# Kernel tuning notes

Hardware: AMD Instinct MI355X
Metric: run time of the kernel (lower is better)

## Reference

```python
import jax, jax.numpy as jnp
import numpy as np

B, P, T = 32, 196, 32           # batch, num pixels (14*14), seq_len
E, H, A, V = 512, 512, 256, 30000  # embed, hidden, attention, vocab
FEAT = 2048

def _ln(x, g, b, eps=1e-5):
    m = jnp.mean(x, -1, keepdims=True)
    v = jnp.mean((x - m) ** 2, -1, keepdims=True)
    return (x - m) / jnp.sqrt(v + eps) * g + b

def setup_inputs() -> dict:
    key = jax.random.key(0)
    ks = iter(jax.random.split(key, 32))
    def rn(shape, s=0.05):
        return (jax.random.normal(next(ks), shape, dtype=jnp.float32) * s)
    inp = {
        'features': jax.random.normal(next(ks), (B, P, FEAT), dtype=jnp.float32),
        'captions': jax.random.randint(next(ks), (B, T), 0, V),
        # feature adapter Linear(2048->E) + LayerNorm
        'Wad': rn((E, FEAT)), 'bad': jnp.zeros((E,), jnp.float32),
        'g_ad': jnp.ones((E,), jnp.float32), 'b_ad': jnp.zeros((E,), jnp.float32),
        # additive attention
        'We': rn((A, E)), 'be': jnp.zeros((A,), jnp.float32),
        'Wd': rn((A, H)), 'bd': jnp.zeros((A,), jnp.float32),
        'Wf': rn((1, A)), 'bf': jnp.zeros((1,), jnp.float32),
        # embedding table (uniform(-0.1,0.1) as in torch init)
        'emb': jax.random.uniform(next(ks), (V, E), jnp.float32, -0.1, 0.1),
        # LSTM layer 0: input 2E, layer 1: input H; gates order i,f,g,o; forget bias 1
        'W_ih0': rn((4 * H, 2 * E)), 'W_hh0': rn((4 * H, H)),
        'b_ih0': jnp.concatenate([jnp.zeros(H), jnp.ones(H), jnp.zeros(2 * H)]).astype(jnp.float32),
        'b_hh0': jnp.zeros((4 * H,), jnp.float32),
        'W_ih1': rn((4 * H, H)), 'W_hh1': rn((4 * H, H)),
        'b_ih1': jnp.concatenate([jnp.zeros(H), jnp.ones(H), jnp.zeros(2 * H)]).astype(jnp.float32),
        'b_hh1': jnp.zeros((4 * H,), jnp.float32),
        # output head
        'W1': rn((H // 2, H)), 'b1': jnp.zeros((H // 2,), jnp.float32),
        'g1': jnp.ones((H // 2,), jnp.float32), 'bb1': jnp.zeros((H // 2,), jnp.float32),
        'W2': rn((V, H // 2)), 'b2': jnp.zeros((V,), jnp.float32),
    }
    return inp

def reference(features, captions, Wad, bad, g_ad, b_ad, We, be, Wd, bd, Wf, bf,
              emb, W_ih0, W_hh0, b_ih0, b_hh0, W_ih1, W_hh1, b_ih1, b_hh1,
              W1, b1, g1, bb1, W2, b2):
    # feature adapter (dropout = identity in eval)
    enc = _ln(jax.nn.relu(features @ Wad.T + bad), g_ad, b_ad)   # [B,P,E]
    att1 = enc @ We.T + be                                        # [B,P,A] (same every step)
    embs = emb[captions]                                          # [B,T,E]

    def lstm_cell(x, h, c, Wih, Whh, bih, bhh):
        gates = x @ Wih.T + bih + h @ Whh.T + bhh                 # [B,4H]
        i, f, g, o = jnp.split(gates, 4, axis=1)
        c_n = jax.nn.sigmoid(f) * c + jax.nn.sigmoid(i) * jnp.tanh(g)
        h_n = jax.nn.sigmoid(o) * jnp.tanh(c_n)
        return h_n, c_n

    def step(carry, emb_t):
        h, c = carry                                              # each [2,B,H]
        # additive attention against top-layer hidden state
        att2 = h[1] @ Wd.T + bd                                   # [B,A]
        e = (jax.nn.relu(att1 + att2[:, None, :]) @ Wf.T + bf)[..., 0]  # [B,P]
        alpha = jax.nn.softmax(e, axis=1)                         # (max-subtract is folded in)
        ctx = jnp.einsum('bp,bpe->be', alpha, enc)                # [B,E]
        x = jnp.concatenate([emb_t, ctx], axis=1)                 # [B,2E]
        h0, c0 = lstm_cell(x,  h[0], c[0], W_ih0, W_hh0, b_ih0, b_hh0)
        h1, c1 = lstm_cell(h0, h[1], c[1], W_ih1, W_hh1, b_ih1, b_hh1)
        out = jax.nn.relu(_ln(h1 @ W1.T + b1, g1, bb1))
        out = jnp.clip(out @ W2.T + b2, -10.0, 10.0)              # [B,V]
        return (jnp.stack([h0, h1]), jnp.stack([c0, c1])), out

    h0 = jnp.zeros((2, B, H), jnp.float32)
    c0 = jnp.zeros((2, B, H), jnp.float32)
    _, outs = jax.lax.scan(step, (h0, c0), jnp.swapaxes(embs, 0, 1))
    return jnp.swapaxes(outs, 0, 1)                               # [B,T,V]
```

## Files before the change

kernel.cpp:

```cpp
#include <hip/hip_runtime.h>

#define B_ 32
#define P_ 196
#define T_ 32
#define E_ 512
#define H_ 512
#define A_ 256
#define V_ 30000
#define FEAT_ 2048

typedef unsigned short u16;
typedef __attribute__((ext_vector_type(8))) short bf16x8;
typedef __attribute__((ext_vector_type(4))) float fx4;

#define MFMA16 __builtin_amdgcn_mfma_f32_16x16x32_bf16

__device__ __forceinline__ u16 f2b(float f){
  unsigned u = __builtin_bit_cast(unsigned, f);
  u += 0x7FFFu + ((u >> 16) & 1u);
  return (u16)(u >> 16);
}
__device__ __forceinline__ float b2f(u16 h){
  unsigned u = ((unsigned)h) << 16;
  return __builtin_bit_cast(float, u);
}
__device__ __forceinline__ float sigm(float x){ return 1.f/(1.f + __expf(-x)); }

#define PREP_BLOCKS 25398
__global__ void k_prep(const float* __restrict__ Wad, const float* __restrict__ We,
                       const float* __restrict__ W1f, const float* __restrict__ W2f,
                       const float* __restrict__ Wd,
                       const float* __restrict__ Wih0, const float* __restrict__ Whh0,
                       const float* __restrict__ Wih1, const float* __restrict__ Whh1,
                       const float* __restrict__ bih0, const float* __restrict__ bhh0,
                       const float* __restrict__ bih1, const float* __restrict__ bhh1,
                       const float* __restrict__ emb, const int* __restrict__ cap,
                       u16* __restrict__ Wad16, u16* __restrict__ We16,
                       u16* __restrict__ W1_16, u16* __restrict__ W2pk,
                       unsigned* __restrict__ Wd2, u16* __restrict__ Wg0pk,
                       u16* __restrict__ W1ppk, float* __restrict__ bias0p,
                       float* __restrict__ bias1p, u16* __restrict__ embs16){
  int bid = blockIdx.x, tid = threadIdx.x;
  if (bid < 12288){
    int eid = bid*256 + tid;
    int j = eid & 7, l = (eid >> 3) & 63, frag = eid >> 9;
    int ks = frag % 12; int rest = frag / 12;
    int kw = rest & 3, q = (rest >> 2) & 3, s = rest >> 4;
    int n = q*512 + s*16 + (l & 15);
    int k = kw*384 + ks*32 + ((l >> 4) << 3) + j;
    float v = (k < 1024) ? Wih0[(size_t)n*1024 + k] : Whh0[(size_t)n*512 + (k - 1024)];
    Wg0pk[eid] = f2b(v);
  } else if (bid < 20480){
    int eid = (bid-12288)*256 + tid;
    int j = eid & 7, l = (eid >> 3) & 63, f = eid >> 9;
    int nf = f & 127, s = f >> 7;
    int np = nf*16 + (l & 15);
    int k = ((l >> 4) << 3) + j;
    int orig = ((np >> 4) & 3)*512 + (np >> 6)*16 + (np & 15);
    float v = (k < 16) ? Wih1[(size_t)orig*512 + s*16 + k]
                       : Whh1[(size_t)orig*512 + s*16 + (k - 16)];
    W1ppk[eid] = f2b(v);
  } else if (bid < 24230){
    int i = (bid-20480)*256 + tid;
    int l = i & 63, kc = (i >> 6) & 7, nf = i >> 9;
    int row = nf*16 + (l & 15);
    int col = kc*32 + (l >> 4)*8;
    const float4* s = (const float4*)(W2f + (size_t)row*256 + col);
    float4 a = s[0], b = s[1];
    ushort4* d = (ushort4*)(W2pk + (size_t)i*8);
    d[0] = make_ushort4(f2b(a.x), f2b(a.y), f2b(a.z), f2b(a.w));
    d[1] = make_ushort4(f2b(b.x), f2b(b.y), f2b(b.z), f2b(b.w));
  } else if (bid < 24742){
    int i = (bid-24230)*256 + tid;
    const float4* s = (const float4*)Wad + (size_t)i*2;
    float4 a = s[0], b = s[1];
    ushort4* d = (ushort4*)Wad16 + (size_t)i*2;
    d[0] = make_ushort4(f2b(a.x), f2b(a.y), f2b(a.z), f2b(a.w));
    d[1] = make_ushort4(f2b(b.x), f2b(b.y), f2b(b.z), f2b(b.w));
  } else if (bid < 24806){
    int i = (bid-24742)*256 + tid;
    const float4* s = (const float4*)We + (size_t)i*2;
    float4 a = s[0], b = s[1];
    ushort4* d = (ushort4*)We16 + (size_t)i*2;
    d[0] = make_ushort4(f2b(a.x), f2b(a.y), f2b(a.z), f2b(a.w));
    d[1] = make_ushort4(f2b(b.x), f2b(b.y), f2b(b.z), f2b(b.w));
  } else if (bid < 24870){
    int i = (bid-24806)*256 + tid;
    const float4* s = (const float4*)W1f + (size_t)i*2;
    float4 a = s[0], b = s[1];
    ushort4* d = (ushort4*)W1_16 + (size_t)i*2;
    d[0] = make_ushort4(f2b(a.x), f2b(a.y), f2b(a.z), f2b(a.w));
    d[1] = make_ushort4(f2b(b.x), f2b(b.y), f2b(b.z), f2b(b.w));
  } else if (bid < 25126){
    int i = (bid-24870)*256 + tid;
    int n = i & 255, kp = i >> 8;
    unsigned lo = f2b(Wd[n*512 + 2*kp]);
    unsigned hi = f2b(Wd[n*512 + 2*kp + 1]);
    Wd2[i] = lo | (hi << 16);
  } else if (bid < 25134){
    int n = (bid-25126)*256 + tid;
    int c = n & 15, q = (n >> 4) & 3, s = n >> 6;
    int orig = q*512 + s*16 + c;
    bias0p[n] = bih0[orig] + bhh0[orig];
  } else if (bid < 25142){
    int n = (bid-25134)*256 + tid;
    int c = n & 15, q = (n >> 4) & 3, s = n >> 6;
    int orig = q*512 + s*16 + c;
    bias1p[n] = bih1[orig] + bhh1[orig];
  } else {
    int r = (bid-25142)*4 + (tid >> 6), l = tid & 63;
    int t = r >> 5, b = r & 31;
    int c = cap[b*T_ + t];
    const float4* s = (const float4*)(emb + (size_t)c*E_) + l*2;
    float4 a = s[0], bb = s[1];
    ushort4* d = (ushort4*)(embs16 + (size_t)r*E_) + l*2;
    d[0] = make_ushort4(f2b(a.x), f2b(a.y), f2b(a.z), f2b(a.w));
    d[1] = make_ushort4(f2b(bb.x), f2b(bb.y), f2b(bb.z), f2b(bb.w));
  }
}

template<int MODE, int BM, int BN, int KS, int NQ>
__launch_bounds__(256)
__global__ void k_gemm(const u16* __restrict__ A, const u16* __restrict__ W,
                       const float* __restrict__ bias, u16* __restrict__ outB,
                       int M, int N, int K){
  constexpr int NI = BN/32, MI = BM/32, SEGS = KS/8;
  __shared__ __align__(16) u16 As[BM][KS+8];
  __shared__ __align__(16) u16 Bs[BN][KS+8];
  int f = blockIdx.x;
  int p8 = f & 7; int rest = f >> 3;
  int q = rest % NQ; int pHigh = rest / NQ;
  int p = pHigh*8 + p8;
  if (p*BM >= M) return;
  int m0 = p*BM, n0 = q*BN;
  int tid = threadIdx.x;
  int l = tid & 63, w = tid >> 6;
  int wr = w >> 1, wc = w & 1;
  fx4 acc[MI][NI];
  #pragma unroll
  for (int i=0;i<MI;i++)
    #pragma unroll
    for (int j=0;j<NI;j++) acc[i][j] = (fx4){0.f,0.f,0.f,0.f};
  int lr = l & 15, lg = l >> 4;
  for (int k0 = 0; k0 < K; k0 += KS){
    #pragma unroll
    for (int it=0; it<BM*SEGS/256; ++it){
      int flat = it*256 + tid, rr = flat/SEGS, cs = (flat%SEGS)*8;
      *(uint4*)&As[rr][cs] = *(const uint4*)(A + (size_t)(m0+rr)*K + k0 + cs);
    }
    uint4 z = {0u,0u,0u,0u};
    #pragma unroll
    for (int it=0; it<BN*SEGS/256; ++it){
      int flat = it*256 + tid, rr = flat/SEGS, cs = (flat%SEGS)*8;
      int rb = n0 + rr;
      *(uint4*)&Bs[rr][cs] = (rb < N) ? *(const uint4*)(W + (size_t)rb*K + k0 + cs) : z;
    }
    __syncthreads();
    #pragma unroll
    for (int kk=0; kk<KS/32; ++kk){
      bf16x8 av[MI], bv[NI];
      #pragma unroll
      for (int mi=0; mi<MI; mi++) av[mi] = *(const bf16x8*)&As[wr*(BM/2) + mi*16 + lr][kk*32 + lg*8];
      #pragma unroll
      for (int ni=0; ni<NI; ni++) bv[ni] = *(const bf16x8*)&Bs[wc*(BN/2) + ni*16 + lr][kk*32 + lg*8];
      #pragma unroll
      for (int mi=0; mi<MI; mi++)
        #pragma unroll
        for (int ni=0; ni<NI; ni++)
          acc[mi][ni] = MFMA16(av[mi], bv[ni], acc[mi][ni], 0, 0, 0);
    }
    __syncthreads();
  }
  #pragma unroll
  for (int mi=0; mi<MI; mi++)
    #pragma unroll
    for (int ni=0; ni<NI; ni++){
      int col = n0 + wc*(BN/2) + ni*16 + lr;
      if (col >= N) continue;
      float bvs = bias[col];
      #pragma unroll
      for (int reg=0; reg<4; reg++){
        int rowm = m0 + wr*(BM/2) + mi*16 + lg*4 + reg;
        float v = acc[mi][ni][reg] + bvs;
        if (MODE == 0) v = fmaxf(v, 0.f);
        outB[(size_t)rowm*N + col] = f2b(v);
      }
    }
}

template<int BM, int BN, int KS, int NQ>
__launch_bounds__(256)
__global__ void k_gemmF(const float* __restrict__ A, const u16* __restrict__ W,
                        const float* __restrict__ bias, u16* __restrict__ outB,
                        int M, int N, int K){
  constexpr int NI = BN/32, MI = BM/32, SEGS = KS/8;
  __shared__ __align__(16) u16 As[BM][KS+8];
  __shared__ __align__(16) u16 Bs[BN][KS+8];
  int f = blockIdx.x;
  int p8 = f & 7; int rest = f >> 3;
  int q = rest % NQ; int pHigh = rest / NQ;
  int p = pHigh*8 + p8;
  if (p*BM >= M) return;
  int m0 = p*BM, n0 = q*BN;
  int tid = threadIdx.x;
  int l = tid & 63, w = tid >> 6;
  int wr = w >> 1, wc = w & 1;
  fx4 acc[MI][NI];
  #pragma unroll
  for (int i=0;i<MI;i++)
    #pragma unroll
    for (int j=0;j<NI;j++) acc[i][j] = (fx4){0.f,0.f,0.f,0.f};
  int lr = l & 15, lg = l >> 4;
  for (int k0 = 0; k0 < K; k0 += KS){
    #pragma unroll
    for (int it=0; it<BM*SEGS/256; ++it){
      int flat = it*256 + tid, rr = flat/SEGS, cs = (flat%SEGS)*8;
      const float4* s = (const float4*)(A + (size_t)(m0+rr)*K + k0 + cs);
      float4 a0 = s[0], a1 = s[1];
      *(ushort4*)&As[rr][cs]   = make_ushort4(f2b(a0.x), f2b(a0.y), f2b(a0.z), f2b(a0.w));
      *(ushort4*)&As[rr][cs+4] = make_ushort4(f2b(a1.x), f2b(a1.y), f2b(a1.z), f2b(a1.w));
    }
    #pragma unroll
    for (int it=0; it<BN*SEGS/256; ++it){
      int flat = it*256 + tid, rr = flat/SEGS, cs = (flat%SEGS)*8;
      *(uint4*)&Bs[rr][cs] = *(const uint4*)(W + (size_t)(n0+rr)*K + k0 + cs);
    }
    __syncthreads();
    #pragma unroll
    for (int kk=0; kk<KS/32; ++kk){
      bf16x8 av[MI], bv[NI];
      #pragma unroll
      for (int mi=0; mi<MI; mi++) av[mi] = *(const bf16x8*)&As[wr*(BM/2) + mi*16 + lr][kk*32 + lg*8];
      #pragma unroll
      for (int ni=0; ni<NI; ni++) bv[ni] = *(const bf16x8*)&Bs[wc*(BN/2) + ni*16 + lr][kk*32 + lg*8];
      #pragma unroll
      for (int mi=0; mi<MI; mi++)
        #pragma unroll
        for (int ni=0; ni<NI; ni++)
          acc[mi][ni] = MFMA16(av[mi], bv[ni], acc[mi][ni], 0, 0, 0);
    }
    __syncthreads();
  }
  #pragma unroll
  for (int mi=0; mi<MI; mi++)
    #pragma unroll
    for (int ni=0; ni<NI; ni++){
      int col = n0 + wc*(BN/2) + ni*16 + lr;
      float bvs = bias[col];
      #pragma unroll
      for (int reg=0; reg<4; reg++){
        int rowm = m0 + wr*(BM/2) + mi*16 + lg*4 + reg;
        float v = fmaxf(acc[mi][ni][reg] + bvs, 0.f);
        outB[(size_t)rowm*N + col] = f2b(v);
      }
    }
}

__global__ void k_ln1(const u16* __restrict__ pre, const float* __restrict__ g,
                      const float* __restrict__ bt, u16* __restrict__ enc){
  int row = blockIdx.x; int l = threadIdx.x;
  bf16x8 vv = *(const bf16x8*)(pre + (size_t)row*E_ + l*8);
  float x[8]; float s = 0.f;
  #pragma unroll
  for (int i=0;i<8;i++){ x[i] = b2f((u16)vv[i]); s += x[i]; }
  #pragma unroll
  for (int off=32; off; off>>=1) s += __shfl_xor(s, off, 64);
  float mean = s * (1.f/512.f);
  float vs = 0.f;
  #pragma unroll
  for (int i=0;i<8;i++){ float d = x[i]-mean; vs += d*d; }
  #pragma unroll
  for (int off=32; off; off>>=1) vs += __shfl_xor(vs, off, 64);
  float inv = rsqrtf(vs*(1.f/512.f) + 1e-5f);
  int c0 = l*8;
  u16 o[8];
  #pragma unroll
  for (int i=0;i<8;i++) o[i] = f2b((x[i]-mean)*inv*g[c0+i] + bt[c0+i]);
  ushort4* d = (ushort4*)(enc + (size_t)row*E_ + c0);
  d[0] = make_ushort4(o[0],o[1],o[2],o[3]);
  d[1] = make_ushort4(o[4],o[5],o[6],o[7]);
}

__device__ __forceinline__ void w1ln_block(const u16* __restrict__ h1all,
    const u16* __restrict__ W1, const float* __restrict__ b1,
    const float* __restrict__ g1v, const float* __restrict__ bb1,
    u16* __restrict__ hid, int u, int tid, float* red2, float* mv){
  int l = tid & 63, w = tid >> 6, lr = l & 15, lg = l >> 4;
  fx4 acc[2] = {{0,0,0,0},{0,0,0,0}};
  for (int k0 = 0; k0 < 512; k0 += 32){
    bf16x8 bv  = *(const bf16x8*)(W1 + (size_t)(w*16+lr)*512 + k0 + lg*8);
    bf16x8 av0 = *(const bf16x8*)(h1all + ((size_t)lr*T_ + u)*512 + k0 + lg*8);
    bf16x8 av1 = *(const bf16x8*)(h1all + ((size_t)(16+lr)*T_ + u)*512 + k0 + lg*8);
    acc[0] = MFMA16(av0, bv, acc[0], 0,0,0);
    acc[1] = MFMA16(av1, bv, acc[1], 0,0,0);
  }
  int col = w*16 + lr;
  float bc = b1[col];
  float val[2][4], s1[2][4], s2[2][4];
  #pragma unroll
  for (int mi=0;mi<2;mi++)
    #pragma unroll
    for (int reg=0;reg<4;reg++){
      float v = acc[mi][reg] + bc;
      val[mi][reg] = v; s1[mi][reg] = v; s2[mi][reg] = v*v;
    }
  #pragma unroll
  for (int off=1; off<16; off<<=1){
    #pragma unroll
    for (int mi=0;mi<2;mi++)
      #pragma unroll
      for (int reg=0;reg<4;reg++){
        s1[mi][reg] += __shfl_xor(s1[mi][reg], off, 64);
        s2[mi][reg] += __shfl_xor(s2[mi][reg], off, 64);
      }
  }
  if (lr == 0){
    #pragma unroll
    for (int mi=0;mi<2;mi++)
      #pragma unroll
      for (int reg=0;reg<4;reg++){
        int row = mi*16 + lg*4 + reg;
        red2[(0*16 + w)*32 + row] = s1[mi][reg];
        red2[(16   + w)*32 + row] = s2[mi][reg];
      }
  }
  __syncthreads();
  if (tid < 64){
    int which = tid >> 5, row = tid & 31;
    float s = 0.f;
    #pragma unroll
    for (int ww=0; ww<16; ++ww) s += red2[(which*16 + ww)*32 + row];
    mv[which*32 + row] = s;
  }
  __syncthreads();
  #pragma unroll
  for (int mi=0;mi<2;mi++)
    #pragma unroll
    for (int reg=0;reg<4;reg++){
      int row = mi*16 + lg*4 + reg;
      float mean = mv[row] * (1.f/256.f);
      float var  = mv[32+row] * (1.f/256.f) - mean*mean;
      float inv  = rsqrtf(var + 1e-5f);
      float o = fmaxf((val[mi][reg]-mean)*inv*g1v[col] + bb1[col], 0.f);
      hid[((size_t)u*32 + row)*256 + col] = f2b(o);
    }
}

__launch_bounds__(1024)
__global__ void k_w1(const u16* __restrict__ h1all, const u16* __restrict__ W1_16,
                     const float* __restrict__ b1, const float* __restrict__ g1v,
                     const float* __restrict__ bb1, u16* __restrict__ hid16){
  __shared__ float red2[1024];
  __shared__ float mv[64];
  w1ln_block(h1all, W1_16, b1, g1v, bb1, hid16, blockIdx.x, threadIdx.x, red2, mv);
}

__launch_bounds__(1024)
__global__ void k_head(const u16* __restrict__ hid, const u16* __restrict__ W2pk,
                       const float* __restrict__ b2, float* __restrict__ out){
  __shared__ __align__(16) union { u16 hA[32][264]; float Cs[32][260]; } S;
  int c = blockIdx.x, uh = blockIdx.y, tid = threadIdx.x;
  int l = tid & 63, w = tid >> 6, lr = l & 15, lg = l >> 4;
  int nf = c*16 + w;
  bool valid = nf < 1875;
  bf16x8 bw[8];
  if (valid){
    const u16* wp = W2pk + (size_t)nf*4096 + l*8;
    #pragma unroll
    for (int k0=0;k0<8;k0++) bw[k0] = *(const bf16x8*)(wp + k0*512);
  }
  int srow = tid >> 5, scc = (tid & 31)*8;
  int col0 = c*256 + scc;
  float bb[8];
  #pragma unroll
  for (int j=0;j<8;j++) bb[j] = (col0 + j < V_) ? b2[col0 + j] : 0.f;

  for (int ui=0; ui<16; ++ui){
    int u = uh*16 + ui;
    { int arow = tid >> 5, ak = (tid & 31)*8;
      *(uint4*)&S.hA[arow][ak] = *(const uint4*)(hid + ((size_t)u*32 + arow)*256 + ak); }
    __syncthreads();
    fx4 acc0 = {0,0,0,0}, acc1 = {0,0,0,0};
    if (valid){
      #pragma unroll
      for (int k0=0;k0<8;k0++){
        bf16x8 av0 = *(const bf16x8*)&S.hA[lr][k0*32 + lg*8];
        bf16x8 av1 = *(const bf16x8*)&S.hA[16+lr][k0*32 + lg*8];
        acc0 = MFMA16(av0, bw[k0], acc0, 0,0,0);
        acc1 = MFMA16(av1, bw[k0], acc1, 0,0,0);
      }
    }
    __syncthreads();
    #pragma unroll
    for (int reg=0; reg<4; ++reg){
      S.Cs[lg*4+reg][w*16+lr]    = acc0[reg];
      S.Cs[16+lg*4+reg][w*16+lr] = acc1[reg];
    }
    __syncthreads();
    if (col0 + 8 <= V_){
      float4 v0, v1;
      v0.x = fminf(fmaxf(S.Cs[srow][scc+0] + bb[0], -10.f), 10.f);
      v0.y = fminf(fmaxf(S.Cs[srow][scc+1] + bb[1], -10.f), 10.f);
      v0.z = fminf(fmaxf(S.Cs[srow][scc+2] + bb[2], -10.f), 10.f);
      v0.w = fminf(fmaxf(S.Cs[srow][scc+3] + bb[3], -10.f), 10.f);
      v1.x = fminf(fmaxf(S.Cs[srow][scc+4] + bb[4], -10.f), 10.f);
      v1.y = fminf(fmaxf(S.Cs[srow][scc+5] + bb[5], -10.f), 10.f);
      v1.z = fminf(fmaxf(S.Cs[srow][scc+6] + bb[6], -10.f), 10.f);
      v1.w = fminf(fmaxf(S.Cs[srow][scc+7] + bb[7], -10.f), 10.f);
      float* o = out + ((size_t)srow*T_ + u)*V_ + col0;
      *(float4*)o = v0; *(float4*)(o+4) = v1;
    }
    __syncthreads();
  }
}

__launch_bounds__(1024)
__global__ void k_ly(const float* __restrict__ part1, const float* __restrict__ bias1p,
                     float* __restrict__ c1buf, u16* __restrict__ h1all,
                     const unsigned* __restrict__ Wd2, const float* __restrict__ bd,
                     const u16* __restrict__ att1b, const u16* __restrict__ enc16,
                     const float* __restrict__ Wf, const float* __restrict__ bfp,
                     const u16* __restrict__ embs, u16* __restrict__ xh0cur, int t){
  int b = blockIdx.x, tid = threadIdx.x;
  int l = tid & 63, wid = tid >> 6;
  __shared__ float g1s[2048];
  __shared__ float h1s[512];
  __shared__ float a2p[4][256];
  __shared__ float a2[256], ev[256], red[8], wfv[256], bdv[256];
  __shared__ float cb[4][256][2];
  if (tid < 256){ wfv[tid] = Wf[tid]; bdv[tid] = bd[tid]; }
  float bf0 = bfp[0];

  if (t > 0){
    float acc0 = bias1p[tid], acc1 = bias1p[tid + 1024];
    #pragma unroll 4
    for (int s2=0; s2<32; ++s2){
      const float* pp = part1 + ((size_t)(s2*32 + b))*2048;
      acc0 += pp[tid];
      acc1 += pp[tid + 1024];
    }
    g1s[tid] = acc0; g1s[tid + 1024] = acc1;
    __syncthreads();
    if (tid < 512){
      int h = tid, s4 = h >> 4, c = h & 15, base = s4*64 + c;
      float gi = g1s[base], gf = g1s[base+16], gg = g1s[base+32], go = g1s[base+48];
      float cold = c1buf[b*512 + h];
      float cn = sigm(gf)*cold + sigm(gi)*tanhf(gg);
      c1buf[b*512 + h] = cn;
      float hn = sigm(go)*tanhf(cn);
      h1s[h] = hn;
      h1all[((size_t)b*T_ + (t-1))*512 + h] = f2b(hn);
    }
  } else {
    if (tid < 512) h1s[tid] = 0.f;
  }
  __syncthreads();
  if (t >= T_) return;

  {
    int n = tid & 255, kq = tid >> 8;
    float acc = 0.f;
    const unsigned* wp = Wd2 + (size_t)kq*64*256 + n;
    #pragma unroll 8
    for (int kp2 = 0; kp2 < 64; ++kp2){
      unsigned wv = wp[(size_t)kp2*256];
      int k0 = (kq*64 + kp2)*2;
      acc += h1s[k0]   * b2f((u16)(wv & 0xFFFFu))
           + h1s[k0+1] * b2f((u16)(wv >> 16));
    }
    a2p[kq][n] = acc;
  }
  __syncthreads();
  if (tid < 256) a2[tid] = a2p[0][tid] + a2p[1][tid] + a2p[2][tid] + a2p[3][tid] + bdv[tid];
  __syncthreads();
  for (int pi = 0; pi < 13; ++pi){
    int p = pi*16 + wid;
    if (p < P_){
      ushort4 av4 = *(const ushort4*)(att1b + (size_t)(b*P_ + p)*A_ + l*4);
      int j0 = l*4;
      float sum = fmaxf(b2f(av4.x)+a2[j0],  0.f)*wfv[j0]
                + fmaxf(b2f(av4.y)+a2[j0+1],0.f)*wfv[j0+1]
                + fmaxf(b2f(av4.z)+a2[j0+2],0.f)*wfv[j0+2]
                + fmaxf(b2f(av4.w)+a2[j0+3],0.f)*wfv[j0+3];
      #pragma unroll
      for (int off=32; off; off>>=1) sum += __shfl_xor(sum, off, 64);
      if (l == 0) ev[p] = sum + bf0;
    }
  }
  __syncthreads();
  if (tid < 256){
    float v = (tid < P_) ? ev[tid] : -1e30f;
    float m = v;
    #pragma unroll
    for (int off=32; off; off>>=1) m = fmaxf(m, __shfl_xor(m, off, 64));
    if (l == 0) red[wid] = m;
  }
  __syncthreads();
  float mg = fmaxf(fmaxf(red[0],red[1]), fmaxf(red[2],red[3]));
  if (tid < 256){
    float ex = (tid < P_) ? __expf(ev[tid] - mg) : 0.f;
    float ss = ex;
    #pragma unroll
    for (int off=32; off; off>>=1) ss += __shfl_xor(ss, off, 64);
    if (l == 0) red[4+wid] = ss;
    ev[tid] = ex;
  }
  __syncthreads();
  float inv = 1.f/(red[4]+red[5]+red[6]+red[7]);
  {
    int j = tid & 255, pq = tid >> 8;
    float A0 = 0.f, A1 = 0.f;
    const unsigned* ep = (const unsigned*)enc16 + ((size_t)b*P_ + pq*49)*256 + j;
    #pragma unroll 7
    for (int pi = 0; pi < 49; ++pi){
      unsigned vv = ep[(size_t)pi*256];
      float al = ev[pq*49 + pi];
      A0 += al * b2f((u16)(vv & 0xFFFFu));
      A1 += al * b2f((u16)(vv >> 16));
    }
    cb[pq][j][0] = A0; cb[pq][j][1] = A1;
  }
  __syncthreads();
  if (tid < 256){
    float c0 = (cb[0][tid][0]+cb[1][tid][0]+cb[2][tid][0]+cb[3][tid][0]) * inv;
    float c1 = (cb[0][tid][1]+cb[1][tid][1]+cb[2][tid][1]+cb[3][tid][1]) * inv;
    unsigned o = (unsigned)f2b(c0) | (((unsigned)f2b(c1)) << 16);
    *((unsigned*)(xh0cur + (size_t)b*1536 + 512) + tid) = o;
    ((unsigned*)(xh0cur + (size_t)b*1536))[tid] =
        ((const unsigned*)(embs + (size_t)(t*32+b)*E_))[tid];
  }
}

__launch_bounds__(1024)
__global__ void k_lx(const u16* __restrict__ xh0cur, u16* __restrict__ xh0nxt,
                     const u16* __restrict__ Wg0pk, const float* __restrict__ bias0p,
                     const u16* __restrict__ W1ppk, const u16* __restrict__ h1all,
                     float* __restrict__ c0buf, float* __restrict__ part1, int t){
  __shared__ float part[16][32][16];
  __shared__ float gsum[4][32][16];
  __shared__ __align__(16) u16 As[32][40];
  int tid = threadIdx.x, s = blockIdx.x;
  int l = tid & 63, kw = tid >> 6, lr = l & 15, lg = l >> 4;

  bf16x8 a[2][3];
  #pragma unroll
  for (int mi=0;mi<2;mi++)
    #pragma unroll
    for (int ks=0;ks<3;ks++)
      a[mi][ks] = *(const bf16x8*)(xh0cur + (size_t)(mi*16+lr)*1536 + kw*96 + ks*32 + lg*8);
  for (int q=0;q<4;q++){
    fx4 acc0 = (fx4){0,0,0,0}, acc1 = (fx4){0,0,0,0};
    const u16* wp = Wg0pk + (size_t)(((s*4+q)*4 + (kw>>2))*12 + (kw&3)*3)*512 + l*8;
    #pragma unroll
    for (int ks=0;ks<3;ks++){
      bf16x8 bf8 = *(const bf16x8*)(wp + ks*512);
      acc0 = MFMA16(a[0][ks], bf8, acc0, 0,0,0);
      acc1 = MFMA16(a[1][ks], bf8, acc1, 0,0,0);
    }
    #pragma unroll
    for (int reg=0;reg<4;reg++){
      part[kw][lg*4+reg][lr]    = acc0[reg];
      part[kw][16+lg*4+reg][lr] = acc1[reg];
    }
    __syncthreads();
    if (tid < 512){
      int bb = tid >> 4, c = tid & 15;
      float g = bias0p[s*64 + q*16 + c];
      #pragma unroll
      for (int kw2=0; kw2<16; ++kw2) g += part[kw2][bb][c];
      gsum[q][bb][c] = g;
    }
    __syncthreads();
  }
  if (tid < 256){
    int bb = tid >> 3, kk = (tid & 7)*2;
    unsigned hv = 0;
    if (t > 0) hv = *(const unsigned*)(h1all + ((size_t)bb*T_ + (t-1))*512 + s*16 + kk);
    *(unsigned*)&As[bb][16+kk] = hv;
  }
  if (tid < 512){
    int bb = tid >> 4, c = tid & 15;
    int h = s*16 + c;
    float gi = gsum[0][bb][c], gf = gsum[1][bb][c], gg = gsum[2][bb][c], go = gsum[3][bb][c];
    float cold = c0buf[bb*512 + h];
    float cn = sigm(gf)*cold + sigm(gi)*tanhf(gg);
    c0buf[bb*512 + h] = cn;
    u16 hb = f2b(sigm(go)*tanhf(cn));
    xh0nxt[(size_t)bb*1536 + 1024 + h] = hb;
    As[bb][c] = hb;
  }
  __syncthreads();
  bf16x8 pa0 = *(const bf16x8*)&As[lr][lg*8];
  bf16x8 pa1 = *(const bf16x8*)&As[16+lr][lg*8];
  #pragma unroll 2
  for (int i=0;i<8;i++){
    int nf = kw*8 + i;
    bf16x8 bf8 = *(const bf16x8*)(W1ppk + (size_t)(s*128 + nf)*512 + l*8);
    fx4 A0 = MFMA16(pa0, bf8, (fx4){0,0,0,0}, 0,0,0);
    fx4 A1 = MFMA16(pa1, bf8, (fx4){0,0,0,0}, 0,0,0);
    float* o = part1 + ((size_t)s*32)*2048 + nf*16 + lr;
    #pragma unroll
    for (int reg=0;reg<4;reg++){
      o[(size_t)(lg*4+reg)*2048]    = A0[reg];
      o[(size_t)(16+lg*4+reg)*2048] = A1[reg];
    }
  }
}

extern "C" void kernel_launch(void* const* d_in, const int* in_sizes, int n_in,
                              void* d_out, int out_size, void* d_ws, size_t ws_size,
                              hipStream_t stream){
  (void)in_sizes; (void)n_in; (void)out_size; (void)ws_size;
  const float* features = (const float*)d_in[0];
  const int*   captions = (const int*)d_in[1];
  const float* Wad  = (const float*)d_in[2];
  const float* bad  = (const float*)d_in[3];
  const float* g_ad = (const float*)d_in[4];
  const float* b_ad = (const float*)d_in[5];
  const float* We   = (const float*)d_in[6];
  const float* be   = (const float*)d_in[7];
  const float* Wd   = (const float*)d_in[8];
  const float* bd   = (const float*)d_in[9];
  const float* Wf   = (const float*)d_in[10];
  const float* bfp  = (const float*)d_in[11];
  const float* emb  = (const float*)d_in[12];
  const float* W_ih0 = (const float*)d_in[13];
  const float* W_hh0 = (const float*)d_in[14];
  const float* b_ih0 = (const float*)d_in[15];
  const float* b_hh0 = (const float*)d_in[16];
  const float* W_ih1 = (const float*)d_in[17];
  const float* W_hh1 = (const float*)d_in[18];
  const float* b_ih1 = (const float*)d_in[19];
  const float* b_hh1 = (const float*)d_in[20];
  const float* W1  = (const float*)d_in[21];
  const float* b1  = (const float*)d_in[22];
  const float* g1  = (const float*)d_in[23];
  const float* bb1 = (const float*)d_in[24];
  const float* W2  = (const float*)d_in[25];
  const float* b2  = (const float*)d_in[26];
  float* out = (float*)d_out;

  char* wsb = (char*)d_ws;
  size_t off = 0;
  auto alloc = [&](size_t bytes)->char*{
    char* p = wsb + off; off += (bytes + 255) & ~(size_t)255; return p;
  };
  u16* Wad16   = (u16*)alloc((size_t)512*2048*2);
  u16* We16    = (u16*)alloc((size_t)256*512*2);
  u16* W1_16   = (u16*)alloc((size_t)256*512*2);
  u16* W2pk    = (u16*)alloc((size_t)1875*8*512*2);
  unsigned* Wd2 = (unsigned*)alloc((size_t)256*256*4);
  u16* Wg0pk   = (u16*)alloc((size_t)2048*1536*2);
  u16* W1ppk   = (u16*)alloc((size_t)32*128*512*2);
  float* bias0p = (float*)alloc(2048*4);
  float* bias1p = (float*)alloc(2048*4);
  u16* embs16  = (u16*)alloc((size_t)1024*512*2);
  u16* pre16   = (u16*)alloc((size_t)6272*512*2);
  u16* enc16   = (u16*)alloc((size_t)6272*512*2);
  u16* att1_16 = (u16*)alloc((size_t)6272*256*2);
  u16* xh0     = (u16*)alloc((size_t)2*32*1536*2);
  float* c0buf = (float*)alloc(32*512*4);
  float* c1buf = (float*)alloc(32*512*4);
  float* part1 = (float*)alloc((size_t)32*32*2048*4);
  u16* h1all16 = (u16*)alloc((size_t)1024*512*2);
  u16* hid16   = (u16*)alloc((size_t)1024*256*2);

  hipMemsetAsync(xh0, 0, 196608 + 65536 + 65536, stream);

  k_prep<<<PREP_BLOCKS,256,0,stream>>>(Wad, We, W1, W2, Wd,
                                       W_ih0, W_hh0, W_ih1, W_hh1,
                                       b_ih0, b_hh0, b_ih1, b_hh1,
                                       emb, captions,
                                       Wad16, We16, W1_16, W2pk, Wd2,
                                       Wg0pk, W1ppk, bias0p, bias1p, embs16);

  k_gemmF<64,64,128,8><<<832,256,0,stream>>>(features, Wad16, bad, pre16, 6272, 512, 2048);
  k_ln1<<<6272,64,0,stream>>>(pre16, g_ad, b_ad, enc16);
  k_gemm<1,64,64,64,4><<<416,256,0,stream>>>(enc16, We16, be, att1_16, 6272, 256, 512);

  u16* xb[2] = { xh0, xh0 + 32*1536 };
  for (int t = 0; t < T_; ++t){
    k_ly<<<32,1024,0,stream>>>(part1, bias1p, c1buf, h1all16, Wd2, bd,
                               att1_16, enc16, Wf, bfp, embs16, xb[t&1], t);
    k_lx<<<32,1024,0,stream>>>(xb[t&1], xb[1-(t&1)], Wg0pk, bias0p,
                               W1ppk, h1all16, c0buf, part1, t);
  }
  k_ly<<<32,1024,0,stream>>>(part1, bias1p, c1buf, h1all16, Wd2, bd,
                             att1_16, enc16, Wf, bfp, embs16, xb[0], T_);

  k_w1<<<32,1024,0,stream>>>(h1all16, W1_16, b1, g1, bb1, hid16);
  k_head<<<dim3(118,2),1024,0,stream>>>(hid16, W2pk, b2, out);
}
```

Baseline: 1.333 ms.

## Split LSTM layer-0 kernel across batch halves and pre-convert features to bf16

```diff
diff --git a/kernel.cpp b/kernel.cpp
--- a/kernel.cpp
+++ b/kernel.cpp
@@ -26,7 +26,7 @@
 }
 __device__ __forceinline__ float sigm(float x){ return 1.f/(1.f + __expf(-x)); }
 
-#define PREP_BLOCKS 25398
+#define PREP_BLOCKS 31670
 __global__ void k_prep(const float* __restrict__ Wad, const float* __restrict__ We,
                        const float* __restrict__ W1f, const float* __restrict__ W2f,
                        const float* __restrict__ Wd,
@@ -35,11 +35,13 @@
                        const float* __restrict__ bih0, const float* __restrict__ bhh0,
                        const float* __restrict__ bih1, const float* __restrict__ bhh1,
                        const float* __restrict__ emb, const int* __restrict__ cap,
+                       const float* __restrict__ feat,
                        u16* __restrict__ Wad16, u16* __restrict__ We16,
                        u16* __restrict__ W1_16, u16* __restrict__ W2pk,
                        unsigned* __restrict__ Wd2, u16* __restrict__ Wg0pk,
                        u16* __restrict__ W1ppk, float* __restrict__ bias0p,
-                       float* __restrict__ bias1p, u16* __restrict__ embs16){
+                       float* __restrict__ bias1p, u16* __restrict__ embs16,
+                       u16* __restrict__ fb16){
   int bid = blockIdx.x, tid = threadIdx.x;
   if (bid < 12288){
     int eid = bid*256 + tid;
@@ -107,7 +109,7 @@
     int c = n & 15, q = (n >> 4) & 3, s = n >> 6;
     int orig = q*512 + s*16 + c;
     bias1p[n] = bih1[orig] + bhh1[orig];
-  } else {
+  } else if (bid < 25398){
     int r = (bid-25142)*4 + (tid >> 6), l = tid & 63;
     int t = r >> 5, b = r & 31;
     int c = cap[b*T_ + t];
@@ -116,6 +118,13 @@
     ushort4* d = (ushort4*)(embs16 + (size_t)r*E_) + l*2;
     d[0] = make_ushort4(f2b(a.x), f2b(a.y), f2b(a.z), f2b(a.w));
     d[1] = make_ushort4(f2b(bb.x), f2b(bb.y), f2b(bb.z), f2b(bb.w));
+  } else {
+    int i = (bid-25398)*256 + tid;
+    const float4* s = (const float4*)feat + (size_t)i*2;
+    float4 a = s[0], b = s[1];
+    ushort4* d = (ushort4*)fb16 + (size_t)i*2;
+    d[0] = make_ushort4(f2b(a.x), f2b(a.y), f2b(a.z), f2b(a.w));
+    d[1] = make_ushort4(f2b(b.x), f2b(b.y), f2b(b.z), f2b(b.w));
   }
 }
 
@@ -188,74 +197,6 @@
     }
 }
 
-template<int BM, int BN, int KS, int NQ>
-__launch_bounds__(256)
-__global__ void k_gemmF(const float* __restrict__ A, const u16* __restrict__ W,
-                        const float* __restrict__ bias, u16* __restrict__ outB,
-                        int M, int N, int K){
-  constexpr int NI = BN/32, MI = BM/32, SEGS = KS/8;
-  __shared__ __align__(16) u16 As[BM][KS+8];
-  __shared__ __align__(16) u16 Bs[BN][KS+8];
-  int f = blockIdx.x;
-  int p8 = f & 7; int rest = f >> 3;
-  int q = rest % NQ; int pHigh = rest / NQ;
-  int p = pHigh*8 + p8;
-  if (p*BM >= M) return;
-  int m0 = p*BM, n0 = q*BN;
-  int tid = threadIdx.x;
-  int l = tid & 63, w = tid >> 6;
-  int wr = w >> 1, wc = w & 1;
-  fx4 acc[MI][NI];
-  #pragma unroll
-  for (int i=0;i<MI;i++)
-    #pragma unroll
-    for (int j=0;j<NI;j++) acc[i][j] = (fx4){0.f,0.f,0.f,0.f};
-  int lr = l & 15, lg = l >> 4;
-  for (int k0 = 0; k0 < K; k0 += KS){
-    #pragma unroll
-    for (int it=0; it<BM*SEGS/256; ++it){
-      int flat = it*256 + tid, rr = flat/SEGS, cs = (flat%SEGS)*8;
-      const float4* s = (const float4*)(A + (size_t)(m0+rr)*K + k0 + cs);
-      float4 a0 = s[0], a1 = s[1];
-      *(ushort4*)&As[rr][cs]   = make_ushort4(f2b(a0.x), f2b(a0.y), f2b(a0.z), f2b(a0.w));
-      *(ushort4*)&As[rr][cs+4] = make_ushort4(f2b(a1.x), f2b(a1.y), f2b(a1.z), f2b(a1.w));
-    }
-    #pragma unroll
-    for (int it=0; it<BN*SEGS/256; ++it){
-      int flat = it*256 + tid, rr = flat/SEGS, cs = (flat%SEGS)*8;
-      *(uint4*)&Bs[rr][cs] = *(const uint4*)(W + (size_t)(n0+rr)*K + k0 + cs);
-    }
-    __syncthreads();
-    #pragma unroll
-    for (int kk=0; kk<KS/32; ++kk){
-      bf16x8 av[MI], bv[NI];
-      #pragma unroll
-      for (int mi=0; mi<MI; mi++) av[mi] = *(const bf16x8*)&As[wr*(BM/2) + mi*16 + lr][kk*32 + lg*8];
-      #pragma unroll
-      for (int ni=0; ni<NI; ni++) bv[ni] = *(const bf16x8*)&Bs[wc*(BN/2) + ni*16 + lr][kk*32 + lg*8];
-      #pragma unroll
-      for (int mi=0; mi<MI; mi++)
-        #pragma unroll
-        for (int ni=0; ni<NI; ni++)
-          acc[mi][ni] = MFMA16(av[mi], bv[ni], acc[mi][ni], 0, 0, 0);
-    }
-    __syncthreads();
-  }
-  #pragma unroll
-  for (int mi=0; mi<MI; mi++)
-    #pragma unroll
-    for (int ni=0; ni<NI; ni++){
-      int col = n0 + wc*(BN/2) + ni*16 + lr;
-      float bvs = bias[col];
-      #pragma unroll
-      for (int reg=0; reg<4; reg++){
-        int rowm = m0 + wr*(BM/2) + mi*16 + lg*4 + reg;
-        float v = fmaxf(acc[mi][ni][reg] + bvs, 0.f);
-        outB[(size_t)rowm*N + col] = f2b(v);
-      }
-    }
-}
-
 __global__ void k_ln1(const u16* __restrict__ pre, const float* __restrict__ g,
                       const float* __restrict__ bt, u16* __restrict__ enc){
   int row = blockIdx.x; int l = threadIdx.x;
@@ -536,34 +477,37 @@
                      const u16* __restrict__ Wg0pk, const float* __restrict__ bias0p,
                      const u16* __restrict__ W1ppk, const u16* __restrict__ h1all,
                      float* __restrict__ c0buf, float* __restrict__ part1, int t){
-  __shared__ float part[16][32][16];
-  __shared__ float gsum[4][32][16];
-  __shared__ __align__(16) u16 As[32][40];
-  int tid = threadIdx.x, s = blockIdx.x;
+  __shared__ float part[16][16][16];
+  __shared__ float gsum[4][16][16];
+  __shared__ __align__(16) u16 As[16][40];
+  int tid = threadIdx.x;
+  int s = blockIdx.x >> 1, half = blockIdx.x & 1;
   int l = tid & 63, kw = tid >> 6, lr = l & 15, lg = l >> 4;
-
-  bf16x8 a[2][3];
-  #pragma unroll
-  for (int mi=0;mi<2;mi++)
-    #pragma unroll
-    for (int ks=0;ks<3;ks++)
-      a[mi][ks] = *(const bf16x8*)(xh0cur + (size_t)(mi*16+lr)*1536 + kw*96 + ks*32 + lg*8);
+  int babs = half*16 + lr;
+
+  bf16x8 a[3];
+  #pragma unroll
+  for (int ks=0;ks<3;ks++)
+    a[ks] = *(const bf16x8*)(xh0cur + (size_t)babs*1536 + kw*96 + ks*32 + lg*8);
+  if (tid < 128){
+    int bb = tid >> 3, kk = (tid & 7)*2;
+    unsigned hv = 0;
+    if (t > 0) hv = *(const unsigned*)(h1all + ((size_t)(half*16+bb)*T_ + (t-1))*512 + s*16 + kk);
+    *(unsigned*)&As[bb][16+kk] = hv;
+  }
   for (int q=0;q<4;q++){
-    fx4 acc0 = (fx4){0,0,0,0}, acc1 = (fx4){0,0,0,0};
+    fx4 acc0 = (fx4){0,0,0,0};
     const u16* wp = Wg0pk + (size_t)(((s*4+q)*4 + (kw>>2))*12 + (kw&3)*3)*512 + l*8;
     #pragma unroll
     for (int ks=0;ks<3;ks++){
       bf16x8 bf8 = *(const bf16x8*)(wp + ks*512);
-      acc0 = MFMA16(a[0][ks], bf8, acc0, 0,0,0);
-      acc1 = MFMA16(a[1][ks], bf8, acc1, 0,0,0);
-    }
-    #pragma unroll
-    for (int reg=0;reg<4;reg++){
-      part[kw][lg*4+reg][lr]    = acc0[reg];
-      part[kw][16+lg*4+reg][lr] = acc1[reg];
-    }
-    __syncthreads();
-    if (tid < 512){
+      acc0 = MFMA16(a[ks], bf8, acc0, 0,0,0);
+    }
+    #pragma unroll
+    for (int reg=0;reg<4;reg++)
+      part[kw][lg*4+reg][lr] = acc0[reg];
+    __syncthreads();
+    if (tid < 256){
       int bb = tid >> 4, c = tid & 15;
       float g = bias0p[s*64 + q*16 + c];
       #pragma unroll
@@ -573,37 +517,27 @@
     __syncthreads();
   }
   if (tid < 256){
-    int bb = tid >> 3, kk = (tid & 7)*2;
-    unsigned hv = 0;
-    if (t > 0) hv = *(const unsigned*)(h1all + ((size_t)bb*T_ + (t-1))*512 + s*16 + kk);
-    *(unsigned*)&As[bb][16+kk] = hv;
-  }
-  if (tid < 512){
     int bb = tid >> 4, c = tid & 15;
-    int h = s*16 + c;
+    int h = s*16 + c, ba = half*16 + bb;
     float gi = gsum[0][bb][c], gf = gsum[1][bb][c], gg = gsum[2][bb][c], go = gsum[3][bb][c];
-    float cold = c0buf[bb*512 + h];
+    float cold = c0buf[ba*512 + h];
     float cn = sigm(gf)*cold + sigm(gi)*tanhf(gg);
-    c0buf[bb*512 + h] = cn;
+    c0buf[ba*512 + h] = cn;
     u16 hb = f2b(sigm(go)*tanhf(cn));
-    xh0nxt[(size_t)bb*1536 + 1024 + h] = hb;
+    xh0nxt[(size_t)ba*1536 + 1024 + h] = hb;
     As[bb][c] = hb;
   }
   __syncthreads();
   bf16x8 pa0 = *(const bf16x8*)&As[lr][lg*8];
-  bf16x8 pa1 = *(const bf16x8*)&As[16+lr][lg*8];
   #pragma unroll 2
   for (int i=0;i<8;i++){
     int nf = kw*8 + i;
     bf16x8 bf8 = *(const bf16x8*)(W1ppk + (size_t)(s*128 + nf)*512 + l*8);
     fx4 A0 = MFMA16(pa0, bf8, (fx4){0,0,0,0}, 0,0,0);
-    fx4 A1 = MFMA16(pa1, bf8, (fx4){0,0,0,0}, 0,0,0);
-    float* o = part1 + ((size_t)s*32)*2048 + nf*16 + lr;
-    #pragma unroll
-    for (int reg=0;reg<4;reg++){
-      o[(size_t)(lg*4+reg)*2048]    = A0[reg];
-      o[(size_t)(16+lg*4+reg)*2048] = A1[reg];
-    }
+    float* o = part1 + ((size_t)s*32 + half*16)*2048 + nf*16 + lr;
+    #pragma unroll
+    for (int reg=0;reg<4;reg++)
+      o[(size_t)(lg*4+reg)*2048] = A0[reg];
   }
 }
 
@@ -645,6 +579,7 @@
   auto alloc = [&](size_t bytes)->char*{
     char* p = wsb + off; off += (bytes + 255) & ~(size_t)255; return p;
   };
+  u16* fb16    = (u16*)alloc((size_t)6272*2048*2);
   u16* Wad16   = (u16*)alloc((size_t)512*2048*2);
   u16* We16    = (u16*)alloc((size_t)256*512*2);
   u16* W1_16   = (u16*)alloc((size_t)256*512*2);
@@ -670,11 +605,11 @@
   k_prep<<<PREP_BLOCKS,256,0,stream>>>(Wad, We, W1, W2, Wd,
                                        W_ih0, W_hh0, W_ih1, W_hh1,
                                        b_ih0, b_hh0, b_ih1, b_hh1,
-                                       emb, captions,
+                                       emb, captions, features,
                                        Wad16, We16, W1_16, W2pk, Wd2,
-                                       Wg0pk, W1ppk, bias0p, bias1p, embs16);
-
-  k_gemmF<64,64,128,8><<<832,256,0,stream>>>(features, Wad16, bad, pre16, 6272, 512, 2048);
+                                       Wg0pk, W1ppk, bias0p, bias1p, embs16, fb16);
+
+  k_gemm<0,64,64,64,8><<<832,256,0,stream>>>(fb16, Wad16, bad, pre16, 6272, 512, 2048);
   k_ln1<<<6272,64,0,stream>>>(pre16, g_ad, b_ad, enc16);
   k_gemm<1,64,64,64,4><<<416,256,0,stream>>>(enc16, We16, be, att1_16, 6272, 256, 512);
 
@@ -682,7 +617,7 @@
   for (int t = 0; t < T_; ++t){
     k_ly<<<32,1024,0,stream>>>(part1, bias1p, c1buf, h1all16, Wd2, bd,
                                att1_16, enc16, Wf, bfp, embs16, xb[t&1], t);
-    k_lx<<<32,1024,0,stream>>>(xb[t&1], xb[1-(t&1)], Wg0pk, bias0p,
+    k_lx<<<64,1024,0,stream>>>(xb[t&1], xb[1-(t&1)], Wg0pk, bias0p,
                                W1ppk, h1all16, c0buf, part1, t);
   }
   k_ly<<<32,1024,0,stream>>>(part1, bias1p, c1buf, h1all16, Wd2, bd,
```

Result: faster. 1.244 ms (-6.7%).
